# Performance work log

Hardware: AMD Instinct MI355X
Metric: run time of the kernel (lower is better)

## Reference

```python
import jax, jax.numpy as jnp
import numpy as np

DIM = 256
B, W_IN, H_IN = 8, 96, 96


def setup_inputs() -> dict:
    key = jax.random.key(0)
    k1, k2, k3 = jax.random.split(key, 3)
    x = jax.random.normal(k1, (B, W_IN, H_IN, DIM), dtype=jnp.float32)
    # Conv2d(dim, 3*dim, kernel_size=1): weight (3C, C) (1x1 spatial dropped), bias (3C,)
    w_qkv = jax.random.normal(k2, (3 * DIM, DIM), dtype=jnp.float32) * (1.0 / np.sqrt(DIM))
    b_qkv = jax.random.normal(k3, (3 * DIM,), dtype=jnp.float32) * 0.01
    return {"x": x, "w_qkv": w_qkv, "b_qkv": b_qkv}


def reference(x, w_qkv, b_qkv):
    # x: (B, W, H, C) -> transpose(3,1) -> (B, C, H, W)
    xt = jnp.transpose(x, (0, 3, 2, 1))
    # 1x1 conv == channel GEMM
    qvk = jnp.einsum('bchw,oc->bohw', xt, w_qkv) + b_qkv[None, :, None, None]
    q, k, v = jnp.split(qvk, 3, axis=1)  # each (B, C, H, W)
    Bn, C, H, W = q.shape

    q_t = jnp.transpose(q, (0, 2, 1, 3))            # (B, H, C, W)
    qk = q_t.reshape(Bn, H * C, W)                   # (B, H*C, W)
    qf = q_t.reshape(Bn, H, C * W)                   # (B, H, C*W)
    kq = jnp.transpose(k, (0, 1, 3, 2)).reshape(Bn, C * W, H)  # (B, C*W, H)
    ms = jax.nn.softmax(jnp.matmul(qf, kq), axis=-1)  # (B, H, H) attention over H

    kf = jnp.transpose(k, (0, 3, 2, 1)).reshape(Bn, W, H * C)  # (B, W, H*C)
    ma = jax.nn.softmax(jnp.matmul(kf, qk), axis=-1)  # (B, W, W) attention over W

    vq = jnp.transpose(v, (0, 2, 1, 3)).reshape(Bn, H, C * W)  # (B, H, C*W)
    vk = jnp.transpose(v, (0, 3, 2, 1)).reshape(Bn, W, H * C)  # (B, W, H*C)

    ms = jnp.matmul(ms, vq).reshape(Bn, H, C, W)     # view(B, H, C, W)
    ms = jnp.transpose(ms, (0, 2, 1, 3))             # (B, C, H, W)
    ma = jnp.matmul(ma, vk).reshape(Bn, W, H, C)     # view(B, W, H, C)
    ma = jnp.transpose(ma, (0, 3, 2, 1))             # (B, C, H, W)

    # final transpose(3,1): (B, C, H, W) -> (B, W, H, C)
    return jnp.transpose(ms + ma, (0, 3, 2, 1))
```

## Files before the change

kernel.cpp:

```cpp
#include <hip/hip_runtime.h>
#include <math.h>

#define SQ 96
#define CQ 256
#define OQ 768
#define HWQ 9216
#define PIXQ 73728

typedef __attribute__((ext_vector_type(8))) __bf16 bf16x8;
typedef __attribute__((ext_vector_type(4))) float f32x4;

union FragU { uint4 u; bf16x8 b; };

__device__ inline uint32_t bf16_rne_u(float f) {
  uint32_t u = __float_as_uint(f);
  return (u + 0x7FFFu + ((u >> 16) & 1u)) >> 16;
}
__device__ inline uint32_t pack_split(float f) {
  uint32_t hi = bf16_rne_u(f);
  float rem = f - __uint_as_float(hi << 16);
  uint32_t lo = __float_as_uint(rem) >> 16;
  return hi | (lo << 16);
}
__device__ inline void unpack_frags(uint4 r0, uint4 r1, FragU& hi, FragU& lo) {
  hi.u.x = (r0.x & 0xFFFFu) | (r0.y << 16);
  hi.u.y = (r0.z & 0xFFFFu) | (r0.w << 16);
  hi.u.z = (r1.x & 0xFFFFu) | (r1.y << 16);
  hi.u.w = (r1.z & 0xFFFFu) | (r1.w << 16);
  lo.u.x = (r0.x >> 16) | (r0.y & 0xFFFF0000u);
  lo.u.y = (r0.z >> 16) | (r0.w & 0xFFFF0000u);
  lo.u.z = (r1.x >> 16) | (r1.y & 0xFFFF0000u);
  lo.u.w = (r1.z >> 16) | (r1.w & 0xFFFF0000u);
}

__global__ __launch_bounds__(256) void pack_w_kernel(
    const float* __restrict__ w, uint32_t* __restrict__ wp) {
  int i = blockIdx.x * 256 + threadIdx.x;
  wp[i] = pack_split(w[i]);
}

__global__ __launch_bounds__(256) void qkv_gemm_mfma(
    const float* __restrict__ x, const uint32_t* __restrict__ wp,
    const float* __restrict__ bias, uint32_t* __restrict__ qk,
    ushort* __restrict__ vb) {
  __shared__ uint32_t Apk[128 * 32];
  __shared__ uint32_t Bpk[128 * 32];
  const int tid = threadIdx.x;
  const int lane = tid & 63;
  const int wid = tid >> 6;
  const int wm = wid >> 1, wn = wid & 1;
  const int lr = lane & 15, quad = lane >> 4;
  const int m0 = blockIdx.x * 128, n0 = blockIdx.y * 128;
  const int sr = tid >> 1, skh = (tid & 1) * 16;

  f32x4 acc[4][4] = {};

  for (int k0 = 0; k0 < 256; k0 += 32) {
    const float* xsrc = x + (size_t)(m0 + sr) * 256 + k0 + skh;
    uint32_t* adst = Apk + sr * 32 + skh;
#pragma unroll
    for (int j = 0; j < 4; ++j) {
      float4 v = *(const float4*)(xsrc + 4 * j);
      uint4 p;
      p.x = pack_split(v.x); p.y = pack_split(v.y);
      p.z = pack_split(v.z); p.w = pack_split(v.w);
      *(uint4*)(adst + 4 * j) = p;
    }
    const uint32_t* wsrc = wp + (size_t)(n0 + sr) * 256 + k0 + skh;
    uint32_t* bdst = Bpk + sr * 32 + skh;
#pragma unroll
    for (int j = 0; j < 4; ++j)
      *(uint4*)(bdst + 4 * j) = *(const uint4*)(wsrc + 4 * j);
    __syncthreads();

    FragU ah[4], al[4], bh[4], bl[4];
#pragma unroll
    for (int t = 0; t < 4; ++t) {
      const uint32_t* pa = Apk + (wm * 64 + t * 16 + lr) * 32 + quad * 8;
      unpack_frags(*(const uint4*)pa, *(const uint4*)(pa + 4), ah[t], al[t]);
      const uint32_t* pb = Bpk + (wn * 64 + t * 16 + lr) * 32 + quad * 8;
      unpack_frags(*(const uint4*)pb, *(const uint4*)(pb + 4), bh[t], bl[t]);
    }
#pragma unroll
    for (int i = 0; i < 4; ++i)
#pragma unroll
      for (int j = 0; j < 4; ++j) {
        acc[i][j] = __builtin_amdgcn_mfma_f32_16x16x32_bf16(al[i].b, bl[j].b, acc[i][j], 0, 0, 0);
        acc[i][j] = __builtin_amdgcn_mfma_f32_16x16x32_bf16(al[i].b, bh[j].b, acc[i][j], 0, 0, 0);
        acc[i][j] = __builtin_amdgcn_mfma_f32_16x16x32_bf16(ah[i].b, bl[j].b, acc[i][j], 0, 0, 0);
        acc[i][j] = __builtin_amdgcn_mfma_f32_16x16x32_bf16(ah[i].b, bh[j].b, acc[i][j], 0, 0, 0);
      }
    __syncthreads();
  }

#pragma unroll
  for (int i = 0; i < 4; ++i) {
    const int growb = m0 + wm * 64 + i * 16 + quad * 4;
#pragma unroll
    for (int r = 0; r < 4; ++r) {
      int p = growb + r;
      int b = p / HWQ;
      int rem = p - b * HWQ;
      int ww = rem / SQ;
      int hh = rem - ww * SQ;
      size_t opix = (size_t)b * HWQ + (size_t)hh * SQ + ww;
#pragma unroll
      for (int j = 0; j < 4; ++j) {
        int o = n0 + wn * 64 + j * 16 + lr;
        float val = acc[i][j][r] + bias[o];
        if (o < 512) qk[opix * 512 + o] = pack_split(val);
        else vb[opix * 256 + (o - 512)] = (ushort)bf16_rne_u(val);
      }
    }
  }
}

__global__ __launch_bounds__(256) void attn_scores_mfma(
    const uint32_t* __restrict__ qk, float* __restrict__ Sh,
    float* __restrict__ Sw) {
  __shared__ uint32_t Xpk[96 * 32];
  __shared__ uint32_t Ypk[96 * 32];
  const int tid = threadIdx.x;
  const int lane = tid & 63;
  const int wid = tid >> 6;
  const int wm = wid >> 1, wn = wid & 1;
  const int lr = lane & 15, quad = lane >> 4;
  const int chunk = blockIdx.x;
  const int b = blockIdx.y;
  const int which = blockIdx.z;
  const size_t base = (size_t)b * HWQ * 512;
  const int offX = which ? 256 : 0;
  const int offY = which ? 0 : 256;

  f32x4 acc[3][3] = {};

  for (int it = 0; it < 24; ++it) {
    int kout = chunk * 3 + (it >> 3);
    int c0 = (it & 7) * 32;
#pragma unroll
    for (int j = 0; j < 3; ++j) {
      int s = j * 256 + tid;
      int row = s >> 3;
      int c4 = (s & 7) * 4;
      size_t idx = which ? ((size_t)kout * SQ + row) : ((size_t)row * SQ + kout);
      const uint32_t* src = qk + base + idx * 512 + c0 + c4;
      *(uint4*)(Xpk + row * 32 + c4) = *(const uint4*)(src + offX);
      *(uint4*)(Ypk + row * 32 + c4) = *(const uint4*)(src + offY);
    }
    __syncthreads();
    FragU xh[3], xl[3], yh[3], yl[3];
#pragma unroll
    for (int t = 0; t < 3; ++t) {
      const uint32_t* px = Xpk + (wm * 48 + t * 16 + lr) * 32 + quad * 8;
      unpack_frags(*(const uint4*)px, *(const uint4*)(px + 4), xh[t], xl[t]);
      const uint32_t* py = Ypk + (wn * 48 + t * 16 + lr) * 32 + quad * 8;
      unpack_frags(*(const uint4*)py, *(const uint4*)(py + 4), yh[t], yl[t]);
    }
#pragma unroll
    for (int i = 0; i < 3; ++i)
#pragma unroll
      for (int j = 0; j < 3; ++j) {
        acc[i][j] = __builtin_amdgcn_mfma_f32_16x16x32_bf16(xl[i].b, yl[j].b, acc[i][j], 0, 0, 0);
        acc[i][j] = __builtin_amdgcn_mfma_f32_16x16x32_bf16(xl[i].b, yh[j].b, acc[i][j], 0, 0, 0);
        acc[i][j] = __builtin_amdgcn_mfma_f32_16x16x32_bf16(xh[i].b, yl[j].b, acc[i][j], 0, 0, 0);
        acc[i][j] = __builtin_amdgcn_mfma_f32_16x16x32_bf16(xh[i].b, yh[j].b, acc[i][j], 0, 0, 0);
      }
    __syncthreads();
  }
  float* S = which ? Sw : Sh;
#pragma unroll
  for (int i = 0; i < 3; ++i)
#pragma unroll
    for (int r = 0; r < 4; ++r)
#pragma unroll
      for (int j = 0; j < 3; ++j) {
        int row = wm * 48 + i * 16 + quad * 4 + r;
        int col = wn * 48 + j * 16 + lr;
        atomicAdd(S + ((size_t)b * SQ + row) * SQ + col, acc[i][j][r]);
      }
}

__global__ __launch_bounds__(256) void softmax_p(
    const float* __restrict__ Sh, const float* __restrict__ Sw,
    ushort* __restrict__ Pms, ushort* __restrict__ Pma) {
  const int tid = threadIdx.x;
  const int lane = tid & 63;
  const int row = blockIdx.x * 4 + (tid >> 6);
  const float* p = (row < 768) ? (Sh + (size_t)row * SQ)
                               : (Sw + (size_t)(row - 768) * SQ);
  ushort* q = (row < 768) ? (Pms + (size_t)row * SQ)
                          : (Pma + (size_t)(row - 768) * SQ);
  float v0 = p[lane];
  float v1 = (lane < 32) ? p[64 + lane] : -3.0e38f;
  float m = fmaxf(v0, v1);
#pragma unroll
  for (int off = 32; off > 0; off >>= 1) m = fmaxf(m, __shfl_xor(m, off));
  float e0 = __expf(v0 - m);
  float e1 = (lane < 32) ? __expf(v1 - m) : 0.0f;
  float s = e0 + e1;
#pragma unroll
  for (int off = 32; off > 0; off >>= 1) s += __shfl_xor(s, off);
  float inv = 1.0f / s;
  q[lane] = (ushort)bf16_rne_u(e0 * inv);
  if (lane < 32) q[64 + lane] = (ushort)bf16_rne_u(e1 * inv);
}

__global__ __launch_bounds__(256) void attn_apply_mfma(
    const ushort* __restrict__ vb, const ushort* __restrict__ P,
    float* __restrict__ out, const int which) {
  __shared__ ushort Vt[256 * 40];
  const int tid = threadIdx.x;
  const int lane = tid & 63;
  const int wid = tid >> 6;
  const int wm = wid >> 1, wn = wid & 1;
  const int lr = lane & 15, quad = lane >> 4;
  const int xi = blockIdx.x;
  const int b = blockIdx.y;

  f32x4 acc[3][8] = {};

  for (int k0 = 0; k0 < 96; k0 += 32) {
#pragma unroll
    for (int j = 0; j < 8; ++j) {
      int bi = j * 256 + tid;
      int c2 = bi & 127;
      int k2 = bi >> 7;
      int k = k0 + k2 * 2;
      int c = c2 * 2;
      size_t r0, r1;
      if (which == 0) {
        r0 = ((size_t)b * HWQ + (size_t)k * SQ + xi) * CQ + c;
        r1 = r0 + (size_t)SQ * CQ;
      } else {
        r0 = ((size_t)b * HWQ + (size_t)xi * SQ + k) * CQ + c;
        r1 = r0 + CQ;
      }
      uint32_t a0 = *(const uint32_t*)(vb + r0);
      uint32_t a1 = *(const uint32_t*)(vb + r1);
      uint32_t w0 = (a0 & 0xFFFFu) | (a1 << 16);
      uint32_t w1 = (a0 >> 16) | (a1 & 0xFFFF0000u);
      *(uint32_t*)&Vt[c * 40 + k2 * 2] = w0;
      *(uint32_t*)&Vt[(c + 1) * 40 + k2 * 2] = w1;
    }
    __syncthreads();
    FragU a[3];
#pragma unroll
    for (int t = 0; t < 3; ++t) {
      int row = wm * 48 + t * 16 + lr;
      const ushort* ps = P + ((size_t)b * SQ + row) * SQ + k0 + quad * 8;
      a[t].u = *(const uint4*)ps;
    }
#pragma unroll
    for (int j = 0; j < 8; ++j) {
      int cb = wn * 128 + j * 16 + lr;
      FragU bf;
      bf.u = *(const uint4*)&Vt[cb * 40 + quad * 8];
#pragma unroll
      for (int i = 0; i < 3; ++i)
        acc[i][j] = __builtin_amdgcn_mfma_f32_16x16x32_bf16(a[i].b, bf.b, acc[i][j], 0, 0, 0);
    }
    __syncthreads();
  }

#pragma unroll
  for (int i = 0; i < 3; ++i) {
#pragma unroll
    for (int r = 0; r < 4; ++r) {
      int mrow = wm * 48 + i * 16 + quad * 4 + r;
      size_t obase;
      if (which == 0) obase = (((size_t)b * SQ + xi) * SQ + mrow) * CQ;
      else            obase = (((size_t)b * SQ + mrow) * SQ + xi) * CQ;
#pragma unroll
      for (int j = 0; j < 8; ++j) {
        int c = wn * 128 + j * 16 + lr;
        if (which == 0) out[obase + c] = acc[i][j][r];
        else            out[obase + c] += acc[i][j][r];
      }
    }
  }
}

extern "C" void kernel_launch(void* const* d_in, const int* in_sizes, int n_in,
                              void* d_out, int out_size, void* d_ws,
                              size_t ws_size, hipStream_t stream) {
  const float* x = (const float*)d_in[0];
  const float* w = (const float*)d_in[1];
  const float* bias = (const float*)d_in[2];
  float* out = (float*)d_out;

  uint32_t* qk  = (uint32_t*)d_ws;
  ushort*   vb  = (ushort*)(qk + (size_t)PIXQ * 512);
  float*    Sh  = (float*)(vb + (size_t)PIXQ * 256);
  float*    Sw  = Sh + PIXQ;
  ushort*   Pms = (ushort*)(Sw + PIXQ);
  ushort*   Pma = Pms + PIXQ;
  uint32_t* wp  = (uint32_t*)(Pma + PIXQ);

  hipMemsetAsync(Sh, 0, 2 * (size_t)PIXQ * sizeof(float), stream);

  pack_w_kernel<<<dim3(768), 256, 0, stream>>>(w, wp);
  qkv_gemm_mfma<<<dim3(576, 6), 256, 0, stream>>>(x, wp, bias, qk, vb);
  attn_scores_mfma<<<dim3(32, 8, 2), 256, 0, stream>>>(qk, Sh, Sw);
  softmax_p<<<dim3(384), 256, 0, stream>>>(Sh, Sw, Pms, Pma);
  attn_apply_mfma<<<dim3(96, 8), 256, 0, stream>>>(vb, Pms, out, 0);
  attn_apply_mfma<<<dim3(96, 8), 256, 0, stream>>>(vb, Pma, out, 1);
}
```

Before: 462.4 us.

## Fold Q/K projections into a combined weight and stream split bf16 planes

Scores now come from x times a precomputed Wq^T·Wk matrix instead of materialising Q and K. The bias contributions are folded into rank-one terms (tq/tk) that initialise the score buffers. This cuts the QKV GEMM output from 768 to 512 columns and removes the packed q/k workspace. Inputs are pre-split into separate hi and lo bf16 planes, loaded into swizzled LDS with direct global-to-LDS copies, and the lo×lo MFMA term is dropped, going from 4 to 3 products per tile. It adds several small setup kernels and an extra full pass over x, and it changes rounding behaviour slightly.

```diff
diff --git a/kernel.cpp b/kernel.cpp
--- a/kernel.cpp
+++ b/kernel.cpp
@@ -3,7 +3,6 @@
 
 #define SQ 96
 #define CQ 256
-#define OQ 768
 #define HWQ 9216
 #define PIXQ 73728
 
@@ -22,73 +21,162 @@
   uint32_t lo = __float_as_uint(rem) >> 16;
   return hi | (lo << 16);
 }
-__device__ inline void unpack_frags(uint4 r0, uint4 r1, FragU& hi, FragU& lo) {
-  hi.u.x = (r0.x & 0xFFFFu) | (r0.y << 16);
-  hi.u.y = (r0.z & 0xFFFFu) | (r0.w << 16);
-  hi.u.z = (r1.x & 0xFFFFu) | (r1.y << 16);
-  hi.u.w = (r1.z & 0xFFFFu) | (r1.w << 16);
-  lo.u.x = (r0.x >> 16) | (r0.y & 0xFFFF0000u);
-  lo.u.y = (r0.z >> 16) | (r0.w & 0xFFFF0000u);
-  lo.u.z = (r1.x >> 16) | (r1.y & 0xFFFF0000u);
-  lo.u.w = (r1.z >> 16) | (r1.w & 0xFFFF0000u);
-}
-
-__global__ __launch_bounds__(256) void pack_w_kernel(
-    const float* __restrict__ w, uint32_t* __restrict__ wp) {
-  int i = blockIdx.x * 256 + threadIdx.x;
-  wp[i] = pack_split(w[i]);
-}
-
-__global__ __launch_bounds__(256) void qkv_gemm_mfma(
-    const float* __restrict__ x, const uint32_t* __restrict__ wp,
-    const float* __restrict__ bias, uint32_t* __restrict__ qk,
-    ushort* __restrict__ vb) {
-  __shared__ uint32_t Apk[128 * 32];
-  __shared__ uint32_t Bpk[128 * 32];
+
+__device__ inline void async_copy16(const void* g, void* l) {
+  __builtin_amdgcn_global_load_lds(
+      (const __attribute__((address_space(1))) void*)g,
+      (__attribute__((address_space(3))) void*)l, 16, 0, 0);
+}
+
+__global__ __launch_bounds__(256) void build_wbig(
+    const float* __restrict__ w, ushort* __restrict__ wbhi,
+    ushort* __restrict__ wblo) {
+  const int n = blockIdx.x;
+  const int j = threadIdx.x;
+  float val;
+  if (n < 256) {
+    float acc = 0.0f;
+#pragma unroll 4
+    for (int o = 0; o < 256; ++o)
+      acc = fmaf(w[o * 256 + n], w[(256 + o) * 256 + j], acc);
+    val = acc;
+  } else {
+    val = w[(256 + n) * 256 + j];
+  }
+  uint32_t p = pack_split(val);
+  wbhi[n * 256 + j] = (ushort)p;
+  wblo[n * 256 + j] = (ushort)(p >> 16);
+}
+
+__global__ __launch_bounds__(256) void build_c2c3(
+    const float* __restrict__ w, const float* __restrict__ bias,
+    float* __restrict__ c2, float* __restrict__ c3) {
+  const int c = threadIdx.x;
+  if (blockIdx.x == 0) {
+    float acc = 0.0f;
+#pragma unroll 4
+    for (int o = 0; o < 256; ++o)
+      acc = fmaf(w[(256 + o) * 256 + c], bias[o], acc);
+    c2[c] = acc;
+  } else {
+    float acc = 0.0f;
+#pragma unroll 4
+    for (int o = 0; o < 256; ++o)
+      acc = fmaf(w[o * 256 + c], bias[256 + o], acc);
+    c3[c] = acc;
+  }
+}
+
+__global__ __launch_bounds__(256) void split_x(
+    const float* __restrict__ x, ushort* __restrict__ xhi,
+    ushort* __restrict__ xlo) {
+  size_t i = ((size_t)blockIdx.x * 256 + threadIdx.x) * 4;
+  float4 v = *(const float4*)(x + i);
+  ushort4 h, l;
+  uint32_t p;
+  p = pack_split(v.x); h.x = (ushort)p; l.x = (ushort)(p >> 16);
+  p = pack_split(v.y); h.y = (ushort)p; l.y = (ushort)(p >> 16);
+  p = pack_split(v.z); h.z = (ushort)p; l.z = (ushort)(p >> 16);
+  p = pack_split(v.w); h.w = (ushort)p; l.w = (ushort)(p >> 16);
+  *(ushort4*)(xhi + i) = h;
+  *(ushort4*)(xlo + i) = l;
+}
+
+__global__ __launch_bounds__(256) void build_tqtk(
+    const float* __restrict__ x, const float* __restrict__ c2,
+    const float* __restrict__ c3, float* __restrict__ tq,
+    float* __restrict__ tk) {
+  __shared__ float red[256];
+  const int i = blockIdx.x;
+  const int b = blockIdx.y;
+  const int c = threadIdx.x;
+  float accq = 0.0f, acck = 0.0f;
+  for (int s = 0; s < 96; ++s) {
+    accq += x[(((size_t)b * SQ + s) * SQ + i) * CQ + c];
+    acck += x[(((size_t)b * SQ + i) * SQ + s) * CQ + c];
+  }
+  red[c] = accq * c2[c];
+  __syncthreads();
+  for (int s = 128; s > 0; s >>= 1) {
+    if (c < s) red[c] += red[c + s];
+    __syncthreads();
+  }
+  if (c == 0) tq[b * SQ + i] = red[0];
+  __syncthreads();
+  red[c] = acck * c3[c];
+  __syncthreads();
+  for (int s = 128; s > 0; s >>= 1) {
+    if (c < s) red[c] += red[c + s];
+    __syncthreads();
+  }
+  if (c == 0) tk[b * SQ + i] = red[0];
+}
+
+__global__ __launch_bounds__(128) void init_scores(
+    const float* __restrict__ tq, const float* __restrict__ tk,
+    float* __restrict__ Sh, float* __restrict__ Sw) {
+  const int id = blockIdx.x;
+  const int t = threadIdx.x;
+  if (t >= 96) return;
+  if (id < 768) {
+    int b = id / 96, rr = id - b * 96;
+    Sh[((size_t)(b * SQ + rr)) * SQ + t] = tq[b * SQ + t];
+  } else {
+    int id2 = id - 768;
+    int b = id2 / 96, rr = id2 - b * 96;
+    Sw[((size_t)(b * SQ + rr)) * SQ + t] = tk[b * SQ + t];
+  }
+}
+
+__global__ __launch_bounds__(256) void yv_gemm_mfma(
+    const ushort* __restrict__ xhi, const ushort* __restrict__ xlo,
+    const ushort* __restrict__ wbhi, const ushort* __restrict__ wblo,
+    const float* __restrict__ bias, ushort* __restrict__ yhi,
+    ushort* __restrict__ ylo, ushort* __restrict__ vb) {
+  __shared__ ushort lds[4][128][32];
   const int tid = threadIdx.x;
   const int lane = tid & 63;
   const int wid = tid >> 6;
   const int wm = wid >> 1, wn = wid & 1;
   const int lr = lane & 15, quad = lane >> 4;
   const int m0 = blockIdx.x * 128, n0 = blockIdx.y * 128;
-  const int sr = tid >> 1, skh = (tid & 1) * 16;
+
+  const ushort* gplane = (wid == 0) ? xhi : (wid == 1) ? xlo
+                       : (wid == 2) ? wbhi : wblo;
+  const int rowbase = (wid < 2) ? m0 : n0;
+  const int srow = lane >> 2;
+  const int lc = (lane & 3) ^ ((lane >> 2) & 3) ^ ((lane >> 4) & 3);
+  const int swz = (lr & 3) ^ ((lr >> 2) & 3);
+  const int ca = ((quad ^ swz) * 8);
 
   f32x4 acc[4][4] = {};
 
   for (int k0 = 0; k0 < 256; k0 += 32) {
-    const float* xsrc = x + (size_t)(m0 + sr) * 256 + k0 + skh;
-    uint32_t* adst = Apk + sr * 32 + skh;
-#pragma unroll
-    for (int j = 0; j < 4; ++j) {
-      float4 v = *(const float4*)(xsrc + 4 * j);
-      uint4 p;
-      p.x = pack_split(v.x); p.y = pack_split(v.y);
-      p.z = pack_split(v.z); p.w = pack_split(v.w);
-      *(uint4*)(adst + 4 * j) = p;
-    }
-    const uint32_t* wsrc = wp + (size_t)(n0 + sr) * 256 + k0 + skh;
-    uint32_t* bdst = Bpk + sr * 32 + skh;
-#pragma unroll
-    for (int j = 0; j < 4; ++j)
-      *(uint4*)(bdst + 4 * j) = *(const uint4*)(wsrc + 4 * j);
+#pragma unroll
+    for (int i = 0; i < 8; ++i) {
+      int row = i * 16 + srow;
+      const ushort* g = gplane + (size_t)(rowbase + row) * 256 + k0 + lc * 8;
+      async_copy16(g, &lds[wid][i * 16][0]);
+    }
     __syncthreads();
 
     FragU ah[4], al[4], bh[4], bl[4];
 #pragma unroll
     for (int t = 0; t < 4; ++t) {
-      const uint32_t* pa = Apk + (wm * 64 + t * 16 + lr) * 32 + quad * 8;
-      unpack_frags(*(const uint4*)pa, *(const uint4*)(pa + 4), ah[t], al[t]);
-      const uint32_t* pb = Bpk + (wn * 64 + t * 16 + lr) * 32 + quad * 8;
-      unpack_frags(*(const uint4*)pb, *(const uint4*)(pb + 4), bh[t], bl[t]);
+      int ra = wm * 64 + t * 16 + lr;
+      int rb = wn * 64 + t * 16 + lr;
+      ah[t].u = *(const uint4*)&lds[0][ra][ca];
+      al[t].u = *(const uint4*)&lds[1][ra][ca];
+      bh[t].u = *(const uint4*)&lds[2][rb][ca];
+      bl[t].u = *(const uint4*)&lds[3][rb][ca];
     }
 #pragma unroll
     for (int i = 0; i < 4; ++i)
 #pragma unroll
       for (int j = 0; j < 4; ++j) {
-        acc[i][j] = __builtin_amdgcn_mfma_f32_16x16x32_bf16(al[i].b, bl[j].b, acc[i][j], 0, 0, 0);
+        acc[i][j] = __builtin_amdgcn_mfma_f32_16x16x32_bf16(ah[i].b, bh[j].b, acc[i][j], 0, 0, 0);
+        acc[i][j] = __builtin_amdgcn_mfma_f32_16x16x32_bf16(ah[i].b, bl[j].b, acc[i][j], 0, 0, 0);
         acc[i][j] = __builtin_amdgcn_mfma_f32_16x16x32_bf16(al[i].b, bh[j].b, acc[i][j], 0, 0, 0);
-        acc[i][j] = __builtin_amdgcn_mfma_f32_16x16x32_bf16(ah[i].b, bl[j].b, acc[i][j], 0, 0, 0);
-        acc[i][j] = __builtin_amdgcn_mfma_f32_16x16x32_bf16(ah[i].b, bh[j].b, acc[i][j], 0, 0, 0);
       }
     __syncthreads();
   }
@@ -107,19 +195,24 @@
 #pragma unroll
       for (int j = 0; j < 4; ++j) {
         int o = n0 + wn * 64 + j * 16 + lr;
-        float val = acc[i][j][r] + bias[o];
-        if (o < 512) qk[opix * 512 + o] = pack_split(val);
-        else vb[opix * 256 + (o - 512)] = (ushort)bf16_rne_u(val);
+        if (o < 256) {
+          uint32_t pk = pack_split(acc[i][j][r]);
+          yhi[opix * 256 + o] = (ushort)pk;
+          ylo[opix * 256 + o] = (ushort)(pk >> 16);
+        } else {
+          float val = acc[i][j][r] + bias[256 + o];
+          vb[opix * 256 + (o - 256)] = (ushort)bf16_rne_u(val);
+        }
       }
     }
   }
 }
 
 __global__ __launch_bounds__(256) void attn_scores_mfma(
-    const uint32_t* __restrict__ qk, float* __restrict__ Sh,
-    float* __restrict__ Sw) {
-  __shared__ uint32_t Xpk[96 * 32];
-  __shared__ uint32_t Ypk[96 * 32];
+    const ushort* __restrict__ xhi, const ushort* __restrict__ xlo,
+    const ushort* __restrict__ yhi, const ushort* __restrict__ ylo,
+    float* __restrict__ Sh, float* __restrict__ Sw) {
+  __shared__ ushort lds[4][96][32];
   const int tid = threadIdx.x;
   const int lane = tid & 63;
   const int wid = tid >> 6;
@@ -128,9 +221,19 @@
   const int chunk = blockIdx.x;
   const int b = blockIdx.y;
   const int which = blockIdx.z;
-  const size_t base = (size_t)b * HWQ * 512;
-  const int offX = which ? 256 : 0;
-  const int offY = which ? 0 : 256;
+  const size_t pbase = (size_t)b * HWQ;
+
+  const ushort* gp;
+  if (which == 0)
+    gp = (wid == 0) ? xhi : (wid == 1) ? xlo : (wid == 2) ? yhi : ylo;
+  else
+    gp = (wid == 0) ? yhi : (wid == 1) ? ylo : (wid == 2) ? xhi : xlo;
+  const bool xop = (wid < 2);
+
+  const int srow = lane >> 2;
+  const int lc = (lane & 3) ^ ((lane >> 2) & 3) ^ ((lane >> 4) & 3);
+  const int swz = (lr & 3) ^ ((lr >> 2) & 3);
+  const int ca = ((quad ^ swz) * 8);
 
   f32x4 acc[3][3] = {};
 
@@ -138,32 +241,31 @@
     int kout = chunk * 3 + (it >> 3);
     int c0 = (it & 7) * 32;
 #pragma unroll
-    for (int j = 0; j < 3; ++j) {
-      int s = j * 256 + tid;
-      int row = s >> 3;
-      int c4 = (s & 7) * 4;
-      size_t idx = which ? ((size_t)kout * SQ + row) : ((size_t)row * SQ + kout);
-      const uint32_t* src = qk + base + idx * 512 + c0 + c4;
-      *(uint4*)(Xpk + row * 32 + c4) = *(const uint4*)(src + offX);
-      *(uint4*)(Ypk + row * 32 + c4) = *(const uint4*)(src + offY);
-    }
-    __syncthreads();
+    for (int i = 0; i < 6; ++i) {
+      int row = i * 16 + srow;
+      size_t pix = xop ? (pbase + (size_t)kout * SQ + row)
+                       : (pbase + (size_t)row * SQ + kout);
+      async_copy16(gp + pix * 256 + c0 + lc * 8, &lds[wid][i * 16][0]);
+    }
+    __syncthreads();
+
     FragU xh[3], xl[3], yh[3], yl[3];
 #pragma unroll
     for (int t = 0; t < 3; ++t) {
-      const uint32_t* px = Xpk + (wm * 48 + t * 16 + lr) * 32 + quad * 8;
-      unpack_frags(*(const uint4*)px, *(const uint4*)(px + 4), xh[t], xl[t]);
-      const uint32_t* py = Ypk + (wn * 48 + t * 16 + lr) * 32 + quad * 8;
-      unpack_frags(*(const uint4*)py, *(const uint4*)(py + 4), yh[t], yl[t]);
+      int rx = wm * 48 + t * 16 + lr;
+      int ry = wn * 48 + t * 16 + lr;
+      xh[t].u = *(const uint4*)&lds[0][rx][ca];
+      xl[t].u = *(const uint4*)&lds[1][rx][ca];
+      yh[t].u = *(const uint4*)&lds[2][ry][ca];
+      yl[t].u = *(const uint4*)&lds[3][ry][ca];
     }
 #pragma unroll
     for (int i = 0; i < 3; ++i)
 #pragma unroll
       for (int j = 0; j < 3; ++j) {
-        acc[i][j] = __builtin_amdgcn_mfma_f32_16x16x32_bf16(xl[i].b, yl[j].b, acc[i][j], 0, 0, 0);
+        acc[i][j] = __builtin_amdgcn_mfma_f32_16x16x32_bf16(xh[i].b, yh[j].b, acc[i][j], 0, 0, 0);
+        acc[i][j] = __builtin_amdgcn_mfma_f32_16x16x32_bf16(xh[i].b, yl[j].b, acc[i][j], 0, 0, 0);
         acc[i][j] = __builtin_amdgcn_mfma_f32_16x16x32_bf16(xl[i].b, yh[j].b, acc[i][j], 0, 0, 0);
-        acc[i][j] = __builtin_amdgcn_mfma_f32_16x16x32_bf16(xh[i].b, yl[j].b, acc[i][j], 0, 0, 0);
-        acc[i][j] = __builtin_amdgcn_mfma_f32_16x16x32_bf16(xh[i].b, yh[j].b, acc[i][j], 0, 0, 0);
       }
     __syncthreads();
   }
@@ -288,19 +390,31 @@
   const float* bias = (const float*)d_in[2];
   float* out = (float*)d_out;
 
-  uint32_t* qk  = (uint32_t*)d_ws;
-  ushort*   vb  = (ushort*)(qk + (size_t)PIXQ * 512);
-  float*    Sh  = (float*)(vb + (size_t)PIXQ * 256);
-  float*    Sw  = Sh + PIXQ;
-  ushort*   Pms = (ushort*)(Sw + PIXQ);
-  ushort*   Pma = Pms + PIXQ;
-  uint32_t* wp  = (uint32_t*)(Pma + PIXQ);
-
-  hipMemsetAsync(Sh, 0, 2 * (size_t)PIXQ * sizeof(float), stream);
-
-  pack_w_kernel<<<dim3(768), 256, 0, stream>>>(w, wp);
-  qkv_gemm_mfma<<<dim3(576, 6), 256, 0, stream>>>(x, wp, bias, qk, vb);
-  attn_scores_mfma<<<dim3(32, 8, 2), 256, 0, stream>>>(qk, Sh, Sw);
+  ushort* xhi = (ushort*)d_ws;
+  ushort* xlo = xhi + (size_t)PIXQ * 256;
+  ushort* yhi = xlo + (size_t)PIXQ * 256;
+  ushort* ylo = yhi + (size_t)PIXQ * 256;
+  ushort* vb  = ylo + (size_t)PIXQ * 256;
+  float*  Sh  = (float*)(vb + (size_t)PIXQ * 256);
+  float*  Sw  = Sh + PIXQ;
+  ushort* Pms = (ushort*)(Sw + PIXQ);
+  ushort* Pma = Pms + PIXQ;
+  ushort* wbhi = Pma + PIXQ;
+  ushort* wblo = wbhi + 512 * 256;
+  float*  c2  = (float*)(wblo + 512 * 256);
+  float*  c3  = c2 + 256;
+  float*  tq  = c3 + 256;
+  float*  tk  = tq + 768;
+
+  build_wbig<<<dim3(512), 256, 0, stream>>>(w, wbhi, wblo);
+  build_c2c3<<<dim3(2), 256, 0, stream>>>(w, bias, c2, c3);
+  split_x<<<dim3(18432), 256, 0, stream>>>(x, xhi, xlo);
+  build_tqtk<<<dim3(96, 8), 256, 0, stream>>>(x, c2, c3, tq, tk);
+  init_scores<<<dim3(1536), 128, 0, stream>>>(tq, tk, Sh, Sw);
+  yv_gemm_mfma<<<dim3(576, 4), 256, 0, stream>>>(xhi, xlo, wbhi, wblo, bias,
+                                                 yhi, ylo, vb);
+  attn_scores_mfma<<<dim3(32, 8, 2), 256, 0, stream>>>(xhi, xlo, yhi, ylo,
+                                                       Sh, Sw);
   softmax_p<<<dim3(384), 256, 0, stream>>>(Sh, Sw, Pms, Pma);
   attn_apply_mfma<<<dim3(96, 8), 256, 0, stream>>>(vb, Pms, out, 0);
   attn_apply_mfma<<<dim3(96, 8), 256, 0, stream>>>(vb, Pma, out, 1);
```

After: 490.7 us. +6.1%, slower.
